# Kernel optimization log

Hardware: AMD Instinct MI355X
Metric: run time of the kernel (lower is better)

The kernel has to match this reference:

```python
import jax, jax.numpy as jnp
import numpy as np

INPUT_SIZE, HIDDEN_SIZE, OUTPUT_SIZE, NUM_LAYERS = 64, 128, 32, 2
B, T = 256, 1024


def setup_inputs() -> dict:
    key = jax.random.key(0)
    ks = jax.random.split(key, 12)
    s = 1.0 / np.sqrt(HIDDEN_SIZE)  # PyTorch LSTM init range
    x = jax.random.normal(ks[0], (B, T, INPUT_SIZE), dtype=jnp.float32)
    h0 = jnp.zeros((NUM_LAYERS, B, HIDDEN_SIZE), dtype=jnp.float32)
    c0 = jnp.zeros((NUM_LAYERS, B, HIDDEN_SIZE), dtype=jnp.float32)
    # layer 0: input -> hidden; layer 1: hidden -> hidden. Gate order i,f,g,o (PyTorch).
    W_ih0 = jax.random.uniform(ks[1], (4 * HIDDEN_SIZE, INPUT_SIZE), minval=-s, maxval=s)
    W_hh0 = jax.random.uniform(ks[2], (4 * HIDDEN_SIZE, HIDDEN_SIZE), minval=-s, maxval=s)
    b_ih0 = jax.random.uniform(ks[3], (4 * HIDDEN_SIZE,), minval=-s, maxval=s)
    b_hh0 = jax.random.uniform(ks[4], (4 * HIDDEN_SIZE,), minval=-s, maxval=s)
    W_ih1 = jax.random.uniform(ks[5], (4 * HIDDEN_SIZE, HIDDEN_SIZE), minval=-s, maxval=s)
    W_hh1 = jax.random.uniform(ks[6], (4 * HIDDEN_SIZE, HIDDEN_SIZE), minval=-s, maxval=s)
    b_ih1 = jax.random.uniform(ks[7], (4 * HIDDEN_SIZE,), minval=-s, maxval=s)
    b_hh1 = jax.random.uniform(ks[8], (4 * HIDDEN_SIZE,), minval=-s, maxval=s)
    fc_w = jax.random.uniform(ks[9], (OUTPUT_SIZE, HIDDEN_SIZE), minval=-s, maxval=s)
    fc_b = jax.random.uniform(ks[10], (OUTPUT_SIZE,), minval=-s, maxval=s)
    return dict(x=x, h0=h0, c0=c0,
                W_ih0=W_ih0, W_hh0=W_hh0, b_ih0=b_ih0, b_hh0=b_hh0,
                W_ih1=W_ih1, W_hh1=W_hh1, b_ih1=b_ih1, b_hh1=b_hh1,
                fc_w=fc_w, fc_b=fc_b)


def _lstm_layer(x_btf, h0, c0, W_ih, W_hh, b_ih, b_hh):
    """x_btf: [B,T,F] -> (out [B,T,H], hT [B,H], cT [B,H]). PyTorch gate order i,f,g,o."""
    H = h0.shape[-1]
    # Precompute input contribution for all timesteps as one big GEMM.
    xp = jnp.einsum('btf,gf->btg', x_btf, W_ih) + b_ih + b_hh  # [B,T,4H]
    xp = jnp.swapaxes(xp, 0, 1)  # time-major [T,B,4H]

    def step(carry, xp_t):
        h, c = carry
        gates = xp_t + h @ W_hh.T  # [B,4H]
        i = jax.nn.sigmoid(gates[:, 0 * H:1 * H])
        f = jax.nn.sigmoid(gates[:, 1 * H:2 * H])
        g = jnp.tanh(gates[:, 2 * H:3 * H])
        o = jax.nn.sigmoid(gates[:, 3 * H:4 * H])
        c = f * c + i * g
        h = o * jnp.tanh(c)
        return (h, c), h

    (hT, cT), hs = jax.lax.scan(step, (h0, c0), xp)
    return jnp.swapaxes(hs, 0, 1), hT, cT  # back to batch_first


def reference(x, h0, c0, W_ih0, W_hh0, b_ih0, b_hh0,
              W_ih1, W_hh1, b_ih1, b_hh1, fc_w, fc_b):
    out0, h_0, c_0 = _lstm_layer(x, h0[0], c0[0], W_ih0, W_hh0, b_ih0, b_hh0)
    out1, h_1, c_1 = _lstm_layer(out0, h0[1], c0[1], W_ih1, W_hh1, b_ih1, b_hh1)
    out = jnp.einsum('bth,oh->bto', out1, fc_w) + fc_b  # [B,T,output_size]
    hN = jnp.stack([h_0, h_1])  # [num_layers,B,H]
    cN = jnp.stack([c_0, c_1])
    return out, hN, cN
```

## Files before the change

### kernel.cpp

```cpp
#include <hip/hip_runtime.h>


static constexpr int B   = 256;
static constexpr int T   = 1024;
static constexpr int H   = 128;
static constexpr int O   = 32;
static constexpr int R   = 4;
static constexpr int NBL = B / R;
static constexpr int CH  = 8;
static constexpr int NCH = T / CH;

static constexpr int HROW = H + 8;
static constexpr int HB   = 0;
static constexpr int HH   = HB + 2 * 16 * HROW;
static constexpr int XB   = HH + 2 * 16 * HROW;
static constexpr int AX   = XB + 2 * 16 * HROW;
static constexpr int AXB  = 8 * 520 + 8;
static constexpr int LDSN = AX + 4 * AXB;

typedef __attribute__((ext_vector_type(8))) short  short8;
typedef __attribute__((ext_vector_type(4))) float  f32x4;

#define LOG2E 1.4426950408889634f

#if __has_builtin(__builtin_amdgcn_exp2f)
#define EXP2(x) __builtin_amdgcn_exp2f(x)
#else
#define EXP2(x) __expf((x) * 0.69314718056f)
#endif
#if __has_builtin(__builtin_amdgcn_rcpf)
#define RCP(x) __builtin_amdgcn_rcpf(x)
#else
#define RCP(x) (1.0f / (x))
#endif

__device__ __forceinline__ unsigned short f2bf(float f) {
  unsigned int u = __builtin_bit_cast(unsigned int, f);
  u += 0x7fffu + ((u >> 16) & 1u);
  return (unsigned short)(u >> 16);
}
__device__ __forceinline__ float bf2f(unsigned short s) {
  return __builtin_bit_cast(float, (unsigned int)s << 16);
}

__device__ __forceinline__ float sigm(float x) {
  return RCP(1.0f + EXP2(-LOG2E * x));
}
__device__ __forceinline__ float tanh_f(float x) {
  return 1.0f - 2.0f * RCP(1.0f + EXP2(2.0f * LOG2E * x));
}

__device__ __forceinline__ void block_sync_lds() {
  __builtin_amdgcn_sched_barrier(0);
  asm volatile("s_waitcnt lgkmcnt(0)" ::: "memory");
  __builtin_amdgcn_s_barrier();
  __builtin_amdgcn_sched_barrier(0);
}

template <int KIN, bool IN_BF16, bool WRITE_HOUT, bool FUSE_FC, bool PROD, bool CONS>
__device__ __forceinline__ void scan_body(
    unsigned short* __restrict__ S,
    const void* __restrict__ in_,
    const float* __restrict__ h0,
    const float* __restrict__ c0,
    const float* __restrict__ Wih,
    const float* __restrict__ Whh,
    const float* __restrict__ bih,
    const float* __restrict__ bhh,
    unsigned short* __restrict__ hout,
    float* __restrict__ hN,
    float* __restrict__ cN,
    const float* __restrict__ Wfc,
    const float* __restrict__ bfc,
    float* __restrict__ fco,
    int* __restrict__ flag, const int bbase)
{
  constexpr int KCX  = KIN / 32;
  constexpr int KCH  = H / 32;
  constexpr int XROW = KIN + 8;

  const int tid  = threadIdx.x;
  const int w    = tid >> 6;
  const int l    = tid & 63;
  const int l15  = l & 15;
  const int lhi  = l >> 4;
  const int jcol = w * 16 + l15;

  short8 wfx[4][KCX], wfh[4][KCH];
  float  bias4[4];
#pragma unroll
  for (int gb = 0; gb < 4; ++gb) {
    const int gc = gb * H + jcol;
    const float* wi = Wih + (size_t)gc * KIN;
    const float* wh = Whh + (size_t)gc * H;
#pragma unroll
    for (int kc = 0; kc < KCX; ++kc) {
      const float* s = wi + kc * 32 + lhi * 8;
      float4 a = *(const float4*)s;
      float4 b = *(const float4*)(s + 4);
      short8 v;
      v[0] = (short)f2bf(a.x); v[1] = (short)f2bf(a.y);
      v[2] = (short)f2bf(a.z); v[3] = (short)f2bf(a.w);
      v[4] = (short)f2bf(b.x); v[5] = (short)f2bf(b.y);
      v[6] = (short)f2bf(b.z); v[7] = (short)f2bf(b.w);
      wfx[gb][kc] = v;
    }
#pragma unroll
    for (int kc = 0; kc < KCH; ++kc) {
      const float* s = wh + kc * 32 + lhi * 8;
      float4 a = *(const float4*)s;
      float4 b = *(const float4*)(s + 4);
      short8 v;
      v[0] = (short)f2bf(a.x); v[1] = (short)f2bf(a.y);
      v[2] = (short)f2bf(a.z); v[3] = (short)f2bf(a.w);
      v[4] = (short)f2bf(b.x); v[5] = (short)f2bf(b.y);
      v[6] = (short)f2bf(b.z); v[7] = (short)f2bf(b.w);
      wfh[gb][kc] = v;
    }
    bias4[gb] = bih[gc] + bhh[gc];
  }

  short8 bfr[4];
  float fcbias = 0.f;
  if constexpr (FUSE_FC) {
    const int oc = (w & 1) * 16 + l15;
#pragma unroll
    for (int kc = 0; kc < 4; ++kc) {
      const float* s = Wfc + (size_t)oc * H + kc * 32 + lhi * 8;
      float4 a = *(const float4*)s;
      float4 b = *(const float4*)(s + 4);
      short8 v;
      v[0] = (short)f2bf(a.x); v[1] = (short)f2bf(a.y);
      v[2] = (short)f2bf(a.z); v[3] = (short)f2bf(a.w);
      v[4] = (short)f2bf(b.x); v[5] = (short)f2bf(b.y);
      v[6] = (short)f2bf(b.z); v[7] = (short)f2bf(b.w);
      bfr[kc] = v;
    }
    fcbias = bfc[oc];
  }

  float cst   = c0[(size_t)(bbase + lhi) * H + jcol];
  float hlast = 0.f;

  const float*          inf = (const float*)in_;
  const unsigned short* inb = (const unsigned short*)in_;

  const int sq  = tid >> 8;
  const int srw = (tid >> 4) & 15;
  const int sb  = bbase + sq * 2 + (srw >> 3);
  const int sts = srw & 7;
  const float*          xsf = inf + ((size_t)sb * T + sts) * KIN + (tid & 15) * 4;
  const unsigned short* xsb = inb + ((size_t)sb * T + sts) * KIN + (tid & 15) * 8;
  const int xdst = XB + (sq * 16 + srw) * XROW +
                   (IN_BF16 ? (tid & 15) * 8 : (tid & 15) * 4);

  unsigned short* hp = nullptr;
  if constexpr (WRITE_HOUT)
    hp = hout + (size_t)(bbase + lhi) * T * H + jcol;

  for (int i = tid; i < 2 * 16 * HROW / 2; i += 512)
    ((unsigned int*)S)[i] = 0u;
  __syncthreads();

  if constexpr (CONS) {
    if (tid == 0) {
      while (__hip_atomic_load(flag, __ATOMIC_ACQUIRE, __HIP_MEMORY_SCOPE_AGENT) < 2)
        __builtin_amdgcn_s_sleep(4);
    }
    __syncthreads();
  }

  if constexpr (IN_BF16) {
    uint4 v = *(const uint4*)xsb;
    *(uint4*)&S[xdst] = v;
  } else {
    float4 v = *(const float4*)xsf;
    uint2 p;
    p.x = (unsigned int)f2bf(v.x) | ((unsigned int)f2bf(v.y) << 16);
    p.y = (unsigned int)f2bf(v.z) | ((unsigned int)f2bf(v.w) << 16);
    *(uint2*)&S[xdst] = p;
  }
  S[HB + (lhi * 4) * HROW + jcol] = f2bf(h0[(size_t)(bbase + lhi) * H + jcol]);
  __syncthreads();

  int cur = 0;
  for (int k = 0; k < NCH; ++k) {
    if constexpr (CONS) {
      if (k > 0) {
        const int want = (k + 2 > NCH) ? NCH : (k + 2);
        if (tid == 0) {
          while (__hip_atomic_load(flag, __ATOMIC_ACQUIRE, __HIP_MEMORY_SCOPE_AGENT) < want)
            __builtin_amdgcn_s_sleep(4);
        }
        __syncthreads();
      }
    }

#pragma unroll
    for (int q = 0; q < 2; ++q) {
      short8 afx[KCX];
#pragma unroll
      for (int kc = 0; kc < KCX; ++kc)
        afx[kc] = *(const short8*)&S[XB + (q * 16 + l15) * XROW + kc * 32 + lhi * 8];
#pragma unroll
      for (int gb = 0; gb < 4; ++gb) {
        f32x4 a = {bias4[gb], bias4[gb], bias4[gb], bias4[gb]};
#pragma unroll
        for (int kc = 0; kc < KCX; ++kc)
          a = __builtin_amdgcn_mfma_f32_16x16x32_bf16(afx[kc], wfx[gb][kc], a, 0, 0, 0);
        const int bb = q * 2 + (lhi >> 1);
#pragma unroll
        for (int r = 0; r < 4; ++r) {
          const int ts = (lhi & 1) * 4 + r;
          S[AX + bb * AXB + ts * 520 + gb * 128 + jcol] = f2bf(a[r]);
        }
      }
    }

    float4 sF; uint4 sB;
    for (int tt = 0; tt < CH; ++tt) {
      if (k + 1 < NCH) {
        if (tt == 0) {
          if constexpr (IN_BF16) sB = *(const uint4*)(xsb + (size_t)(k + 1) * CH * KIN);
          else                   sF = *(const float4*)(xsf + (size_t)(k + 1) * CH * KIN);
        } else if (tt == 1) {
          if constexpr (IN_BF16) {
            *(uint4*)&S[xdst] = sB;
          } else {
            uint2 p;
            p.x = (unsigned int)f2bf(sF.x) | ((unsigned int)f2bf(sF.y) << 16);
            p.y = (unsigned int)f2bf(sF.z) | ((unsigned int)f2bf(sF.w) << 16);
            *(uint2*)&S[xdst] = p;
          }
        }
      }

      float ax[4];
#pragma unroll
      for (int gb = 0; gb < 4; ++gb)
        ax[gb] = bf2f(S[AX + lhi * AXB + tt * 520 + gb * 128 + jcol]);

      short8 afh[KCH];
#pragma unroll
      for (int kc = 0; kc < KCH; ++kc)
        afh[kc] = *(const short8*)&S[HB + (cur * 16 + l15) * HROW + kc * 32 + lhi * 8];

      f32x4 acc[4];
#pragma unroll
      for (int gb = 0; gb < 4; ++gb) {
        f32x4 a = {ax[gb], ax[gb], ax[gb], ax[gb]};
#pragma unroll
        for (int kc = 0; kc < KCH; ++kc)
          a = __builtin_amdgcn_mfma_f32_16x16x32_bf16(afh[kc], wfh[gb][kc], a, 0, 0, 0);
        acc[gb] = a;
      }

      const int nxt = cur ^ 1;
      {
        float i_ = sigm(acc[0][0]);
        float f_ = sigm(acc[1][0]);
        float g_ = tanh_f(acc[2][0]);
        float o_ = sigm(acc[3][0]);
        float c_ = f_ * cst + i_ * g_;
        cst = c_;
        float hn = o_ * tanh_f(c_);
        hlast = hn;
        unsigned short hb = f2bf(hn);
        S[HB + (nxt * 16 + lhi * 4) * HROW + jcol] = hb;
        if constexpr (FUSE_FC)
          S[HH + ((lhi >> 1) * 16 + (lhi & 1) * 8 + tt) * HROW + jcol] = hb;
        if constexpr (WRITE_HOUT) { hp[0] = hb; }
      }
      if constexpr (WRITE_HOUT) hp += H;

      block_sync_lds();
      cur = nxt;
    }

    if constexpr (FUSE_FC) {
      if (w < 4) {
        const int q = w >> 1;
        short8 a4[4];
#pragma unroll
        for (int kc = 0; kc < 4; ++kc)
          a4[kc] = *(const short8*)&S[HH + (q * 16 + l15) * HROW + kc * 32 + lhi * 8];
        f32x4 fs = {fcbias, fcbias, fcbias, fcbias};
#pragma unroll
        for (int kc = 0; kc < 4; ++kc)
          fs = __builtin_amdgcn_mfma_f32_16x16x32_bf16(a4[kc], bfr[kc], fs, 0, 0, 0);
        const int brow = bbase + q * 2 + (lhi >> 1);
        const int tb   = k * CH + (lhi & 1) * 4;
#pragma unroll
        for (int r = 0; r < 4; ++r)
          fco[((size_t)brow * T + tb + r) * O + (w & 1) * 16 + l15] = fs[r];
      }
    }

    if constexpr (PROD) {
      __builtin_amdgcn_sched_barrier(0);
      asm volatile("s_waitcnt vmcnt(0)" ::: "memory");
      __builtin_amdgcn_s_barrier();
      if (tid == 0)
        __hip_atomic_store(flag, k + 1, __ATOMIC_RELEASE, __HIP_MEMORY_SCOPE_AGENT);
    }
  }

  hN[(size_t)(bbase + lhi) * H + jcol] = hlast;
  cN[(size_t)(bbase + lhi) * H + jcol] = cst;
}

__global__ __launch_bounds__(512, 2) void lstm_fused(
    const float* __restrict__ x,
    const float* __restrict__ h0, const float* __restrict__ c0,
    const float* __restrict__ Wih0, const float* __restrict__ Whh0,
    const float* __restrict__ bih0, const float* __restrict__ bhh0,
    const float* __restrict__ Wih1, const float* __restrict__ Whh1,
    const float* __restrict__ bih1, const float* __restrict__ bhh1,
    const float* __restrict__ fcw, const float* __restrict__ fcb,
    unsigned short* __restrict__ out0,
    float* __restrict__ out, float* __restrict__ hN, float* __restrict__ cN,
    int* __restrict__ flags)
{
  __shared__ __align__(16) unsigned short S[LDSN];
  const int bid = blockIdx.x;
  if (bid < NBL) {
    scan_body<64, false, true, false, true, false>(
        S, x, h0, c0, Wih0, Whh0, bih0, bhh0,
        out0, hN, cN, nullptr, nullptr, nullptr,
        flags + bid, bid * R);
  } else {
    const int rb = bid - NBL;
    scan_body<128, true, false, true, false, true>(
        S, out0, h0 + B * H, c0 + B * H, Wih1, Whh1, bih1, bhh1,
        nullptr, hN + B * H, cN + B * H, fcw, fcb, out,
        flags + rb, rb * R);
  }
}

extern "C" void kernel_launch(void* const* d_in, const int* in_sizes, int n_in,
                              void* d_out, int out_size, void* d_ws, size_t ws_size,
                              hipStream_t stream) {
  (void)in_sizes; (void)n_in; (void)out_size; (void)ws_size;

  const float* x    = (const float*)d_in[0];
  const float* h0   = (const float*)d_in[1];
  const float* c0   = (const float*)d_in[2];
  const float* Wih0 = (const float*)d_in[3];
  const float* Whh0 = (const float*)d_in[4];
  const float* bih0 = (const float*)d_in[5];
  const float* bhh0 = (const float*)d_in[6];
  const float* Wih1 = (const float*)d_in[7];
  const float* Whh1 = (const float*)d_in[8];
  const float* bih1 = (const float*)d_in[9];
  const float* bhh1 = (const float*)d_in[10];
  const float* fcw  = (const float*)d_in[11];
  const float* fcb  = (const float*)d_in[12];

  int*            flags = (int*)d_ws;
  unsigned short* out0  = (unsigned short*)((char*)d_ws + 1024);

  float* out = (float*)d_out;
  float* hN  = out + (size_t)B * T * O;
  float* cN  = hN + (size_t)2 * B * H;

  hipMemsetAsync(d_ws, 0, 1024, stream);
  lstm_fused<<<2 * NBL, 512, 0, stream>>>(
      x, h0, c0, Wih0, Whh0, bih0, bhh0, Wih1, Whh1, bih1, bhh1,
      fcw, fcb, out0, out, hN, cN, flags);
}
```

Baseline: 713.8 us.

## Assign one batch row per block and double the time chunk

Each block now handles a single batch element instead of four, which launches 512 blocks in place of 128, and the chunk length grows to 16 timesteps. The MFMA M dimension now spans 16 timesteps of one row, and the x staging buffer is double-buffered by chunk parity. The input-projection weights and the FC weights are now reloaded from global memory every chunk, which frees registers. The intent is to shorten the serial per-step critical path and spread work across more CUs, at the cost of idle lanes (only a quarter write h), redundant weight reloads, and more cross-block flag traffic.

```diff
diff --git a/kernel.cpp b/kernel.cpp
--- a/kernel.cpp
+++ b/kernel.cpp
@@ -5,18 +5,17 @@
 static constexpr int T   = 1024;
 static constexpr int H   = 128;
 static constexpr int O   = 32;
-static constexpr int R   = 4;
-static constexpr int NBL = B / R;
-static constexpr int CH  = 8;
+static constexpr int NBL = 256;
+static constexpr int CH  = 16;
 static constexpr int NCH = T / CH;
 
 static constexpr int HROW = H + 8;
 static constexpr int HB   = 0;
 static constexpr int HH   = HB + 2 * 16 * HROW;
-static constexpr int XB   = HH + 2 * 16 * HROW;
-static constexpr int AX   = XB + 2 * 16 * HROW;
-static constexpr int AXB  = 8 * 520 + 8;
-static constexpr int LDSN = AX + 4 * AXB;
+static constexpr int XRM  = 136;
+static constexpr int XB   = HH + 16 * HROW;
+static constexpr int AX   = XB + 2 * 16 * XRM;
+static constexpr int LDSN = AX + 16 * 520 + 8;
 
 typedef __attribute__((ext_vector_type(8))) short  short8;
 typedef __attribute__((ext_vector_type(4))) float  f32x4;
@@ -75,9 +74,8 @@
     float* __restrict__ fco,
     int* __restrict__ flag, const int bbase)
 {
-  constexpr int KCX  = KIN / 32;
-  constexpr int KCH  = H / 32;
-  constexpr int XROW = KIN + 8;
+  constexpr int KCX = KIN / 32;
+  constexpr int KCH = H / 32;
 
   const int tid  = threadIdx.x;
   const int w    = tid >> 6;
@@ -85,26 +83,14 @@
   const int l15  = l & 15;
   const int lhi  = l >> 4;
   const int jcol = w * 16 + l15;
-
-  short8 wfx[4][KCX], wfh[4][KCH];
+  const bool own = (lhi == 0);
+
+  short8 wfh[4][KCH];
   float  bias4[4];
 #pragma unroll
   for (int gb = 0; gb < 4; ++gb) {
     const int gc = gb * H + jcol;
-    const float* wi = Wih + (size_t)gc * KIN;
     const float* wh = Whh + (size_t)gc * H;
-#pragma unroll
-    for (int kc = 0; kc < KCX; ++kc) {
-      const float* s = wi + kc * 32 + lhi * 8;
-      float4 a = *(const float4*)s;
-      float4 b = *(const float4*)(s + 4);
-      short8 v;
-      v[0] = (short)f2bf(a.x); v[1] = (short)f2bf(a.y);
-      v[2] = (short)f2bf(a.z); v[3] = (short)f2bf(a.w);
-      v[4] = (short)f2bf(b.x); v[5] = (short)f2bf(b.y);
-      v[6] = (short)f2bf(b.z); v[7] = (short)f2bf(b.w);
-      wfx[gb][kc] = v;
-    }
 #pragma unroll
     for (int kc = 0; kc < KCH; ++kc) {
       const float* s = wh + kc * 32 + lhi * 8;
@@ -120,70 +106,43 @@
     bias4[gb] = bih[gc] + bhh[gc];
   }
 
-  short8 bfr[4];
-  float fcbias = 0.f;
-  if constexpr (FUSE_FC) {
-    const int oc = (w & 1) * 16 + l15;
-#pragma unroll
-    for (int kc = 0; kc < 4; ++kc) {
-      const float* s = Wfc + (size_t)oc * H + kc * 32 + lhi * 8;
-      float4 a = *(const float4*)s;
-      float4 b = *(const float4*)(s + 4);
-      short8 v;
-      v[0] = (short)f2bf(a.x); v[1] = (short)f2bf(a.y);
-      v[2] = (short)f2bf(a.z); v[3] = (short)f2bf(a.w);
-      v[4] = (short)f2bf(b.x); v[5] = (short)f2bf(b.y);
-      v[6] = (short)f2bf(b.z); v[7] = (short)f2bf(b.w);
-      bfr[kc] = v;
-    }
-    fcbias = bfc[oc];
-  }
-
-  float cst   = c0[(size_t)(bbase + lhi) * H + jcol];
+  float cst   = c0[(size_t)bbase * H + jcol];
   float hlast = 0.f;
 
   const float*          inf = (const float*)in_;
   const unsigned short* inb = (const unsigned short*)in_;
 
-  const int sq  = tid >> 8;
-  const int srw = (tid >> 4) & 15;
-  const int sb  = bbase + sq * 2 + (srw >> 3);
-  const int sts = srw & 7;
-  const float*          xsf = inf + ((size_t)sb * T + sts) * KIN + (tid & 15) * 4;
-  const unsigned short* xsb = inb + ((size_t)sb * T + sts) * KIN + (tid & 15) * 8;
-  const int xdst = XB + (sq * 16 + srw) * XROW +
-                   (IN_BF16 ? (tid & 15) * 8 : (tid & 15) * 4);
+  const int sts   = tid >> 5;
+  const int slane = tid & 31;
+  const float*          xsf = inf + ((size_t)bbase * T + sts) * KIN + slane * 2;
+  const unsigned short* xsb = inb + ((size_t)bbase * T + sts) * KIN + slane * 4;
+  const int xdoff = sts * XRM + (IN_BF16 ? slane * 4 : slane * 2);
 
   unsigned short* hp = nullptr;
   if constexpr (WRITE_HOUT)
-    hp = hout + (size_t)(bbase + lhi) * T * H + jcol;
+    hp = hout + (size_t)bbase * T * H + jcol;
 
   for (int i = tid; i < 2 * 16 * HROW / 2; i += 512)
     ((unsigned int*)S)[i] = 0u;
-  __syncthreads();
 
   if constexpr (CONS) {
     if (tid == 0) {
       while (__hip_atomic_load(flag, __ATOMIC_ACQUIRE, __HIP_MEMORY_SCOPE_AGENT) < 2)
         __builtin_amdgcn_s_sleep(4);
     }
-    __syncthreads();
-  }
+  }
+  __syncthreads();
 
   if constexpr (IN_BF16) {
-    uint4 v = *(const uint4*)xsb;
-    *(uint4*)&S[xdst] = v;
+    *(uint2*)&S[XB + xdoff] = *(const uint2*)xsb;
   } else {
-    float4 v = *(const float4*)xsf;
-    uint2 p;
-    p.x = (unsigned int)f2bf(v.x) | ((unsigned int)f2bf(v.y) << 16);
-    p.y = (unsigned int)f2bf(v.z) | ((unsigned int)f2bf(v.w) << 16);
-    *(uint2*)&S[xdst] = p;
-  }
-  S[HB + (lhi * 4) * HROW + jcol] = f2bf(h0[(size_t)(bbase + lhi) * H + jcol]);
+    float2 v = *(const float2*)xsf;
+    *(unsigned int*)&S[XB + xdoff] =
+        (unsigned int)f2bf(v.x) | ((unsigned int)f2bf(v.y) << 16);
+  }
+  if (own) S[HB + jcol] = f2bf(h0[(size_t)bbase * H + jcol]);
   __syncthreads();
 
-  int cur = 0;
   for (int k = 0; k < NCH; ++k) {
     if constexpr (CONS) {
       if (k > 0) {
@@ -196,41 +155,55 @@
       }
     }
 
-#pragma unroll
-    for (int q = 0; q < 2; ++q) {
+    {
+      short8 wfx[4][KCX];
+#pragma unroll
+      for (int gb = 0; gb < 4; ++gb) {
+        const float* wi = Wih + (size_t)(gb * H + jcol) * KIN;
+#pragma unroll
+        for (int kc = 0; kc < KCX; ++kc) {
+          const float* s = wi + kc * 32 + lhi * 8;
+          float4 a = *(const float4*)s;
+          float4 b = *(const float4*)(s + 4);
+          short8 v;
+          v[0] = (short)f2bf(a.x); v[1] = (short)f2bf(a.y);
+          v[2] = (short)f2bf(a.z); v[3] = (short)f2bf(a.w);
+          v[4] = (short)f2bf(b.x); v[5] = (short)f2bf(b.y);
+          v[6] = (short)f2bf(b.z); v[7] = (short)f2bf(b.w);
+          wfx[gb][kc] = v;
+        }
+      }
       short8 afx[KCX];
 #pragma unroll
       for (int kc = 0; kc < KCX; ++kc)
-        afx[kc] = *(const short8*)&S[XB + (q * 16 + l15) * XROW + kc * 32 + lhi * 8];
+        afx[kc] = *(const short8*)&S[XB + (k & 1) * 16 * XRM + l15 * XRM + kc * 32 + lhi * 8];
 #pragma unroll
       for (int gb = 0; gb < 4; ++gb) {
         f32x4 a = {bias4[gb], bias4[gb], bias4[gb], bias4[gb]};
 #pragma unroll
         for (int kc = 0; kc < KCX; ++kc)
           a = __builtin_amdgcn_mfma_f32_16x16x32_bf16(afx[kc], wfx[gb][kc], a, 0, 0, 0);
-        const int bb = q * 2 + (lhi >> 1);
-#pragma unroll
-        for (int r = 0; r < 4; ++r) {
-          const int ts = (lhi & 1) * 4 + r;
-          S[AX + bb * AXB + ts * 520 + gb * 128 + jcol] = f2bf(a[r]);
-        }
-      }
-    }
-
-    float4 sF; uint4 sB;
+#pragma unroll
+        for (int r = 0; r < 4; ++r)
+          S[AX + (lhi * 4 + r) * 520 + gb * 128 + jcol] = f2bf(a[r]);
+      }
+    }
+    block_sync_lds();
+
+    float2 sF; uint2 sB;
     for (int tt = 0; tt < CH; ++tt) {
+      const int cur = tt & 1, nxt = cur ^ 1;
+
       if (k + 1 < NCH) {
         if (tt == 0) {
-          if constexpr (IN_BF16) sB = *(const uint4*)(xsb + (size_t)(k + 1) * CH * KIN);
-          else                   sF = *(const float4*)(xsf + (size_t)(k + 1) * CH * KIN);
+          if constexpr (IN_BF16) sB = *(const uint2*)(xsb + (size_t)(k + 1) * CH * KIN);
+          else                   sF = *(const float2*)(xsf + (size_t)(k + 1) * CH * KIN);
         } else if (tt == 1) {
           if constexpr (IN_BF16) {
-            *(uint4*)&S[xdst] = sB;
+            *(uint2*)&S[XB + ((k + 1) & 1) * 16 * XRM + xdoff] = sB;
           } else {
-            uint2 p;
-            p.x = (unsigned int)f2bf(sF.x) | ((unsigned int)f2bf(sF.y) << 16);
-            p.y = (unsigned int)f2bf(sF.z) | ((unsigned int)f2bf(sF.w) << 16);
-            *(uint2*)&S[xdst] = p;
+            *(unsigned int*)&S[XB + ((k + 1) & 1) * 16 * XRM + xdoff] =
+                (unsigned int)f2bf(sF.x) | ((unsigned int)f2bf(sF.y) << 16);
           }
         }
       }
@@ -238,7 +211,7 @@
       float ax[4];
 #pragma unroll
       for (int gb = 0; gb < 4; ++gb)
-        ax[gb] = bf2f(S[AX + lhi * AXB + tt * 520 + gb * 128 + jcol]);
+        ax[gb] = bf2f(S[AX + tt * 520 + gb * 128 + jcol]);
 
       short8 afh[KCH];
 #pragma unroll
@@ -255,7 +228,6 @@
         acc[gb] = a;
       }
 
-      const int nxt = cur ^ 1;
       {
         float i_ = sigm(acc[0][0]);
         float f_ = sigm(acc[1][0]);
@@ -266,33 +238,45 @@
         float hn = o_ * tanh_f(c_);
         hlast = hn;
         unsigned short hb = f2bf(hn);
-        S[HB + (nxt * 16 + lhi * 4) * HROW + jcol] = hb;
-        if constexpr (FUSE_FC)
-          S[HH + ((lhi >> 1) * 16 + (lhi & 1) * 8 + tt) * HROW + jcol] = hb;
-        if constexpr (WRITE_HOUT) { hp[0] = hb; }
+        if (own) {
+          S[HB + nxt * 16 * HROW + jcol] = hb;
+          if constexpr (FUSE_FC) S[HH + tt * HROW + jcol] = hb;
+          if constexpr (WRITE_HOUT) hp[0] = hb;
+        }
       }
       if constexpr (WRITE_HOUT) hp += H;
 
       block_sync_lds();
-      cur = nxt;
     }
 
     if constexpr (FUSE_FC) {
-      if (w < 4) {
-        const int q = w >> 1;
+      if (w < 2) {
+        short8 bfr[4];
+        const int oc = w * 16 + l15;
+#pragma unroll
+        for (int kc = 0; kc < 4; ++kc) {
+          const float* s = Wfc + (size_t)oc * H + kc * 32 + lhi * 8;
+          float4 a = *(const float4*)s;
+          float4 b = *(const float4*)(s + 4);
+          short8 v;
+          v[0] = (short)f2bf(a.x); v[1] = (short)f2bf(a.y);
+          v[2] = (short)f2bf(a.z); v[3] = (short)f2bf(a.w);
+          v[4] = (short)f2bf(b.x); v[5] = (short)f2bf(b.y);
+          v[6] = (short)f2bf(b.z); v[7] = (short)f2bf(b.w);
+          bfr[kc] = v;
+        }
+        const float fcb_ = bfc[oc];
         short8 a4[4];
 #pragma unroll
         for (int kc = 0; kc < 4; ++kc)
-          a4[kc] = *(const short8*)&S[HH + (q * 16 + l15) * HROW + kc * 32 + lhi * 8];
-        f32x4 fs = {fcbias, fcbias, fcbias, fcbias};
+          a4[kc] = *(const short8*)&S[HH + l15 * HROW + kc * 32 + lhi * 8];
+        f32x4 fs = {fcb_, fcb_, fcb_, fcb_};
 #pragma unroll
         for (int kc = 0; kc < 4; ++kc)
           fs = __builtin_amdgcn_mfma_f32_16x16x32_bf16(a4[kc], bfr[kc], fs, 0, 0, 0);
-        const int brow = bbase + q * 2 + (lhi >> 1);
-        const int tb   = k * CH + (lhi & 1) * 4;
 #pragma unroll
         for (int r = 0; r < 4; ++r)
-          fco[((size_t)brow * T + tb + r) * O + (w & 1) * 16 + l15] = fs[r];
+          fco[((size_t)bbase * T + k * CH + lhi * 4 + r) * O + w * 16 + l15] = fs[r];
       }
     }
 
@@ -305,8 +289,10 @@
     }
   }
 
-  hN[(size_t)(bbase + lhi) * H + jcol] = hlast;
-  cN[(size_t)(bbase + lhi) * H + jcol] = cst;
+  if (own) {
+    hN[(size_t)bbase * H + jcol] = hlast;
+    cN[(size_t)bbase * H + jcol] = cst;
+  }
 }
 
 __global__ __launch_bounds__(512, 2) void lstm_fused(
@@ -327,13 +313,13 @@
     scan_body<64, false, true, false, true, false>(
         S, x, h0, c0, Wih0, Whh0, bih0, bhh0,
         out0, hN, cN, nullptr, nullptr, nullptr,
-        flags + bid, bid * R);
+        flags + bid, bid);
   } else {
     const int rb = bid - NBL;
     scan_body<128, true, false, true, false, true>(
         S, out0, h0 + B * H, c0 + B * H, Wih1, Whh1, bih1, bhh1,
         nullptr, hN + B * H, cN + B * H, fcw, fcb, out,
-        flags + rb, rb * R);
+        flags + rb, rb);
   }
 }
 
@@ -357,13 +343,13 @@
   const float* fcb  = (const float*)d_in[12];
 
   int*            flags = (int*)d_ws;
-  unsigned short* out0  = (unsigned short*)((char*)d_ws + 1024);
+  unsigned short* out0  = (unsigned short*)((char*)d_ws + 2048);
 
   float* out = (float*)d_out;
   float* hN  = out + (size_t)B * T * O;
   float* cN  = hN + (size_t)2 * B * H;
 
-  hipMemsetAsync(d_ws, 0, 1024, stream);
+  hipMemsetAsync(d_ws, 0, 2048, stream);
   lstm_fused<<<2 * NBL, 512, 0, stream>>>(
       x, h0, c0, Wih0, Whh0, bih0, bhh0, Wih1, Whh1, bih1, bhh1,
       fcw, fcb, out0, out, hN, cN, flags);
```

After: 1.317 ms. 84.5% more time.

## Keep input projection in registers and pipeline next chunk's MFMA into recurrence

Applied to the files above, without the earlier changes.

The chunk length drops from 8 to 4 timesteps, and the input-projection results stay in MFMA accumulator registers instead of round-tripping through an LDS bf16 buffer. The next chunk's input projection is split across timesteps 2 and 3 of the current chunk, so it overlaps the recurrent MFMAs and nonlinearities. The bf16 layer-1 input is read directly from global memory into MFMA fragments rather than staged through LDS. The producer/consumer flag handshake is kept at the same 8-timestep granularity by acting only on every other chunk. This removes LDS traffic and a separate per-chunk projection phase, at the cost of more register pressure and more frequent FC passes.

```diff
diff --git a/kernel.cpp b/kernel.cpp
--- a/kernel.cpp
+++ b/kernel.cpp
@@ -7,16 +7,15 @@
 static constexpr int O   = 32;
 static constexpr int R   = 4;
 static constexpr int NBL = B / R;
-static constexpr int CH  = 8;
+static constexpr int CH  = 4;
 static constexpr int NCH = T / CH;
 
 static constexpr int HROW = H + 8;
 static constexpr int HB   = 0;
 static constexpr int HH   = HB + 2 * 16 * HROW;
-static constexpr int XB   = HH + 2 * 16 * HROW;
-static constexpr int AX   = XB + 2 * 16 * HROW;
-static constexpr int AXB  = 8 * 520 + 8;
-static constexpr int LDSN = AX + 4 * AXB;
+static constexpr int XROW = 72;
+static constexpr int XB   = HH + 16 * HROW;
+static constexpr int LDSN = XB + 2 * 16 * XROW;
 
 typedef __attribute__((ext_vector_type(8))) short  short8;
 typedef __attribute__((ext_vector_type(4))) float  f32x4;
@@ -39,15 +38,23 @@
   u += 0x7fffu + ((u >> 16) & 1u);
   return (unsigned short)(u >> 16);
 }
-__device__ __forceinline__ float bf2f(unsigned short s) {
-  return __builtin_bit_cast(float, (unsigned int)s << 16);
-}
 
 __device__ __forceinline__ float sigm(float x) {
   return RCP(1.0f + EXP2(-LOG2E * x));
 }
 __device__ __forceinline__ float tanh_f(float x) {
   return 1.0f - 2.0f * RCP(1.0f + EXP2(2.0f * LOG2E * x));
+}
+
+__device__ __forceinline__ short8 cvt8(const float* s) {
+  float4 a = *(const float4*)s;
+  float4 b = *(const float4*)(s + 4);
+  short8 v;
+  v[0] = (short)f2bf(a.x); v[1] = (short)f2bf(a.y);
+  v[2] = (short)f2bf(a.z); v[3] = (short)f2bf(a.w);
+  v[4] = (short)f2bf(b.x); v[5] = (short)f2bf(b.y);
+  v[6] = (short)f2bf(b.z); v[7] = (short)f2bf(b.w);
+  return v;
 }
 
 __device__ __forceinline__ void block_sync_lds() {
@@ -75,9 +82,8 @@
     float* __restrict__ fco,
     int* __restrict__ flag, const int bbase)
 {
-  constexpr int KCX  = KIN / 32;
-  constexpr int KCH  = H / 32;
-  constexpr int XROW = KIN + 8;
+  constexpr int KCX = KIN / 32;
+  constexpr int KCH = H / 32;
 
   const int tid  = threadIdx.x;
   const int w    = tid >> 6;
@@ -86,37 +92,17 @@
   const int lhi  = l >> 4;
   const int jcol = w * 16 + l15;
 
-  short8 wfx[4][KCX], wfh[4][KCH];
+  short8 wfh[4][KCH], wfx[4][KCX];
   float  bias4[4];
 #pragma unroll
   for (int gb = 0; gb < 4; ++gb) {
     const int gc = gb * H + jcol;
-    const float* wi = Wih + (size_t)gc * KIN;
-    const float* wh = Whh + (size_t)gc * H;
-#pragma unroll
-    for (int kc = 0; kc < KCX; ++kc) {
-      const float* s = wi + kc * 32 + lhi * 8;
-      float4 a = *(const float4*)s;
-      float4 b = *(const float4*)(s + 4);
-      short8 v;
-      v[0] = (short)f2bf(a.x); v[1] = (short)f2bf(a.y);
-      v[2] = (short)f2bf(a.z); v[3] = (short)f2bf(a.w);
-      v[4] = (short)f2bf(b.x); v[5] = (short)f2bf(b.y);
-      v[6] = (short)f2bf(b.z); v[7] = (short)f2bf(b.w);
-      wfx[gb][kc] = v;
-    }
-#pragma unroll
-    for (int kc = 0; kc < KCH; ++kc) {
-      const float* s = wh + kc * 32 + lhi * 8;
-      float4 a = *(const float4*)s;
-      float4 b = *(const float4*)(s + 4);
-      short8 v;
-      v[0] = (short)f2bf(a.x); v[1] = (short)f2bf(a.y);
-      v[2] = (short)f2bf(a.z); v[3] = (short)f2bf(a.w);
-      v[4] = (short)f2bf(b.x); v[5] = (short)f2bf(b.y);
-      v[6] = (short)f2bf(b.z); v[7] = (short)f2bf(b.w);
-      wfh[gb][kc] = v;
-    }
+#pragma unroll
+    for (int kc = 0; kc < KCX; ++kc)
+      wfx[gb][kc] = cvt8(Wih + (size_t)gc * KIN + kc * 32 + lhi * 8);
+#pragma unroll
+    for (int kc = 0; kc < KCH; ++kc)
+      wfh[gb][kc] = cvt8(Whh + (size_t)gc * H + kc * 32 + lhi * 8);
     bias4[gb] = bih[gc] + bhh[gc];
   }
 
@@ -125,17 +111,8 @@
   if constexpr (FUSE_FC) {
     const int oc = (w & 1) * 16 + l15;
 #pragma unroll
-    for (int kc = 0; kc < 4; ++kc) {
-      const float* s = Wfc + (size_t)oc * H + kc * 32 + lhi * 8;
-      float4 a = *(const float4*)s;
-      float4 b = *(const float4*)(s + 4);
-      short8 v;
-      v[0] = (short)f2bf(a.x); v[1] = (short)f2bf(a.y);
-      v[2] = (short)f2bf(a.z); v[3] = (short)f2bf(a.w);
-      v[4] = (short)f2bf(b.x); v[5] = (short)f2bf(b.y);
-      v[6] = (short)f2bf(b.z); v[7] = (short)f2bf(b.w);
-      bfr[kc] = v;
-    }
+    for (int kc = 0; kc < 4; ++kc)
+      bfr[kc] = cvt8(Wfc + (size_t)oc * H + kc * 32 + lhi * 8);
     fcbias = bfc[oc];
   }
 
@@ -145,14 +122,12 @@
   const float*          inf = (const float*)in_;
   const unsigned short* inb = (const unsigned short*)in_;
 
-  const int sq  = tid >> 8;
-  const int srw = (tid >> 4) & 15;
-  const int sb  = bbase + sq * 2 + (srw >> 3);
-  const int sts = srw & 7;
-  const float*          xsf = inf + ((size_t)sb * T + sts) * KIN + (tid & 15) * 4;
-  const unsigned short* xsb = inb + ((size_t)sb * T + sts) * KIN + (tid & 15) * 8;
-  const int xdst = XB + (sq * 16 + srw) * XROW +
-                   (IN_BF16 ? (tid & 15) * 8 : (tid & 15) * 4);
+  const int srow = tid >> 5, scol = (tid & 31) * 2;
+  const float* xsf =
+      inf + ((size_t)(bbase + (srow >> 2)) * T + (srow & 3)) * KIN + scol;
+
+  const unsigned short* xgb =
+      inb + ((size_t)(bbase + (l15 >> 2)) * T + (l15 & 3)) * KIN + lhi * 8;
 
   unsigned short* hp = nullptr;
   if constexpr (WRITE_HOUT)
@@ -160,33 +135,47 @@
 
   for (int i = tid; i < 2 * 16 * HROW / 2; i += 512)
     ((unsigned int*)S)[i] = 0u;
-  __syncthreads();
 
   if constexpr (CONS) {
     if (tid == 0) {
       while (__hip_atomic_load(flag, __ATOMIC_ACQUIRE, __HIP_MEMORY_SCOPE_AGENT) < 2)
         __builtin_amdgcn_s_sleep(4);
     }
-    __syncthreads();
-  }
-
-  if constexpr (IN_BF16) {
-    uint4 v = *(const uint4*)xsb;
-    *(uint4*)&S[xdst] = v;
-  } else {
-    float4 v = *(const float4*)xsf;
-    uint2 p;
-    p.x = (unsigned int)f2bf(v.x) | ((unsigned int)f2bf(v.y) << 16);
-    p.y = (unsigned int)f2bf(v.z) | ((unsigned int)f2bf(v.w) << 16);
-    *(uint2*)&S[xdst] = p;
-  }
+  }
+  __syncthreads();
+
   S[HB + (lhi * 4) * HROW + jcol] = f2bf(h0[(size_t)(bbase + lhi) * H + jcol]);
+  if constexpr (!IN_BF16) {
+    float2 v = *(const float2*)xsf;
+    *(unsigned int*)&S[XB + srow * XROW + scol] =
+        (unsigned int)f2bf(v.x) | ((unsigned int)f2bf(v.y) << 16);
+  }
   __syncthreads();
 
-  int cur = 0;
+  f32x4 axc[4];
+  {
+    short8 afx[KCX];
+#pragma unroll
+    for (int kc = 0; kc < KCX; ++kc) {
+      if constexpr (IN_BF16)
+        afx[kc] = *(const short8*)(xgb + kc * 32);
+      else
+        afx[kc] = *(const short8*)&S[XB + l15 * XROW + kc * 32 + lhi * 8];
+    }
+#pragma unroll
+    for (int gb = 0; gb < 4; ++gb) {
+      f32x4 a = {bias4[gb], bias4[gb], bias4[gb], bias4[gb]};
+#pragma unroll
+      for (int kc = 0; kc < KCX; ++kc)
+        a = __builtin_amdgcn_mfma_f32_16x16x32_bf16(afx[kc], wfx[gb][kc], a, 0, 0, 0);
+      axc[gb] = a;
+    }
+  }
+  __syncthreads();
+
   for (int k = 0; k < NCH; ++k) {
     if constexpr (CONS) {
-      if (k > 0) {
+      if (k > 0 && (k & 1) == 0) {
         const int want = (k + 2 > NCH) ? NCH : (k + 2);
         if (tid == 0) {
           while (__hip_atomic_load(flag, __ATOMIC_ACQUIRE, __HIP_MEMORY_SCOPE_AGENT) < want)
@@ -196,49 +185,20 @@
       }
     }
 
-#pragma unroll
-    for (int q = 0; q < 2; ++q) {
-      short8 afx[KCX];
-#pragma unroll
-      for (int kc = 0; kc < KCX; ++kc)
-        afx[kc] = *(const short8*)&S[XB + (q * 16 + l15) * XROW + kc * 32 + lhi * 8];
-#pragma unroll
-      for (int gb = 0; gb < 4; ++gb) {
-        f32x4 a = {bias4[gb], bias4[gb], bias4[gb], bias4[gb]};
-#pragma unroll
-        for (int kc = 0; kc < KCX; ++kc)
-          a = __builtin_amdgcn_mfma_f32_16x16x32_bf16(afx[kc], wfx[gb][kc], a, 0, 0, 0);
-        const int bb = q * 2 + (lhi >> 1);
-#pragma unroll
-        for (int r = 0; r < 4; ++r) {
-          const int ts = (lhi & 1) * 4 + r;
-          S[AX + bb * AXB + ts * 520 + gb * 128 + jcol] = f2bf(a[r]);
-        }
-      }
-    }
-
-    float4 sF; uint4 sB;
+    const bool hasN = (k + 1 < NCH);
+    f32x4 axn[4];
+    float2 pf = {0.f, 0.f};
+
+#pragma unroll
     for (int tt = 0; tt < CH; ++tt) {
-      if (k + 1 < NCH) {
-        if (tt == 0) {
-          if constexpr (IN_BF16) sB = *(const uint4*)(xsb + (size_t)(k + 1) * CH * KIN);
-          else                   sF = *(const float4*)(xsf + (size_t)(k + 1) * CH * KIN);
-        } else if (tt == 1) {
-          if constexpr (IN_BF16) {
-            *(uint4*)&S[xdst] = sB;
-          } else {
-            uint2 p;
-            p.x = (unsigned int)f2bf(sF.x) | ((unsigned int)f2bf(sF.y) << 16);
-            p.y = (unsigned int)f2bf(sF.z) | ((unsigned int)f2bf(sF.w) << 16);
-            *(uint2*)&S[xdst] = p;
-          }
-        }
-      }
-
-      float ax[4];
-#pragma unroll
-      for (int gb = 0; gb < 4; ++gb)
-        ax[gb] = bf2f(S[AX + lhi * AXB + tt * 520 + gb * 128 + jcol]);
+      const int cur = tt & 1, nxt = cur ^ 1;
+
+      if constexpr (!IN_BF16) {
+        if (tt == 0 && hasN) pf = *(const float2*)(xsf + (size_t)(k + 1) * CH * KIN);
+        if (tt == 1 && hasN)
+          *(unsigned int*)&S[XB + ((k + 1) & 1) * 16 * XROW + srow * XROW + scol] =
+              (unsigned int)f2bf(pf.x) | ((unsigned int)f2bf(pf.y) << 16);
+      }
 
       short8 afh[KCH];
 #pragma unroll
@@ -248,14 +208,48 @@
       f32x4 acc[4];
 #pragma unroll
       for (int gb = 0; gb < 4; ++gb) {
-        f32x4 a = {ax[gb], ax[gb], ax[gb], ax[gb]};
+        const float ax = axc[gb][tt];
+        f32x4 a = {ax, ax, ax, ax};
 #pragma unroll
         for (int kc = 0; kc < KCH; ++kc)
           a = __builtin_amdgcn_mfma_f32_16x16x32_bf16(afh[kc], wfh[gb][kc], a, 0, 0, 0);
         acc[gb] = a;
       }
 
-      const int nxt = cur ^ 1;
+      if (tt == 2 && hasN) {
+        short8 afx[2];
+#pragma unroll
+        for (int kc = 0; kc < 2; ++kc) {
+          if constexpr (IN_BF16)
+            afx[kc] = *(const short8*)(xgb + (size_t)(k + 1) * CH * KIN + kc * 32);
+          else
+            afx[kc] = *(const short8*)&S[XB + ((k + 1) & 1) * 16 * XROW +
+                                         l15 * XROW + kc * 32 + lhi * 8];
+        }
+#pragma unroll
+        for (int gb = 0; gb < 4; ++gb) {
+          f32x4 a = {bias4[gb], bias4[gb], bias4[gb], bias4[gb]};
+          a = __builtin_amdgcn_mfma_f32_16x16x32_bf16(afx[0], wfx[gb][0], a, 0, 0, 0);
+          a = __builtin_amdgcn_mfma_f32_16x16x32_bf16(afx[1], wfx[gb][1], a, 0, 0, 0);
+          axn[gb] = a;
+        }
+      }
+      if constexpr (KCX == 4) {
+        if (tt == 3 && hasN) {
+          short8 afx[2];
+#pragma unroll
+          for (int kc = 0; kc < 2; ++kc)
+            afx[kc] = *(const short8*)(xgb + (size_t)(k + 1) * CH * KIN + (2 + kc) * 32);
+#pragma unroll
+          for (int gb = 0; gb < 4; ++gb) {
+            f32x4 a = axn[gb];
+            a = __builtin_amdgcn_mfma_f32_16x16x32_bf16(afx[0], wfx[gb][2], a, 0, 0, 0);
+            a = __builtin_amdgcn_mfma_f32_16x16x32_bf16(afx[1], wfx[gb][3], a, 0, 0, 0);
+            axn[gb] = a;
+          }
+        }
+      }
+
       {
         float i_ = sigm(acc[0][0]);
         float f_ = sigm(acc[1][0]);
@@ -268,40 +262,42 @@
         unsigned short hb = f2bf(hn);
         S[HB + (nxt * 16 + lhi * 4) * HROW + jcol] = hb;
         if constexpr (FUSE_FC)
-          S[HH + ((lhi >> 1) * 16 + (lhi & 1) * 8 + tt) * HROW + jcol] = hb;
-        if constexpr (WRITE_HOUT) { hp[0] = hb; }
-      }
-      if constexpr (WRITE_HOUT) hp += H;
+          S[HH + ((lhi << 2) | tt) * HROW + jcol] = hb;
+        if constexpr (WRITE_HOUT) { hp[0] = hb; hp += H; }
+      }
 
       block_sync_lds();
-      cur = nxt;
     }
 
     if constexpr (FUSE_FC) {
-      if (w < 4) {
-        const int q = w >> 1;
+      if (w < 2) {
         short8 a4[4];
 #pragma unroll
         for (int kc = 0; kc < 4; ++kc)
-          a4[kc] = *(const short8*)&S[HH + (q * 16 + l15) * HROW + kc * 32 + lhi * 8];
+          a4[kc] = *(const short8*)&S[HH + l15 * HROW + kc * 32 + lhi * 8];
         f32x4 fs = {fcbias, fcbias, fcbias, fcbias};
 #pragma unroll
         for (int kc = 0; kc < 4; ++kc)
           fs = __builtin_amdgcn_mfma_f32_16x16x32_bf16(a4[kc], bfr[kc], fs, 0, 0, 0);
-        const int brow = bbase + q * 2 + (lhi >> 1);
-        const int tb   = k * CH + (lhi & 1) * 4;
 #pragma unroll
         for (int r = 0; r < 4; ++r)
-          fco[((size_t)brow * T + tb + r) * O + (w & 1) * 16 + l15] = fs[r];
-      }
+          fco[((size_t)(bbase + lhi) * T + k * CH + r) * O + w * 16 + l15] = fs[r];
+      }
+    }
+
+    if (hasN) {
+#pragma unroll
+      for (int gb = 0; gb < 4; ++gb) axc[gb] = axn[gb];
     }
 
     if constexpr (PROD) {
-      __builtin_amdgcn_sched_barrier(0);
-      asm volatile("s_waitcnt vmcnt(0)" ::: "memory");
-      __builtin_amdgcn_s_barrier();
-      if (tid == 0)
-        __hip_atomic_store(flag, k + 1, __ATOMIC_RELEASE, __HIP_MEMORY_SCOPE_AGENT);
+      if (k & 1) {
+        __builtin_amdgcn_sched_barrier(0);
+        asm volatile("s_waitcnt vmcnt(0)" ::: "memory");
+        __builtin_amdgcn_s_barrier();
+        if (tid == 0)
+          __hip_atomic_store(flag, k + 1, __ATOMIC_RELEASE, __HIP_MEMORY_SCOPE_AGENT);
+      }
     }
   }
 
```

Result: slower. 893.7 us (+25.2%).
